# Kernel tuning notes

Hardware: AMD Instinct MI355X
Metric: run time of the kernel (lower is better)

Reference implementation:

```python
import jax, jax.numpy as jnp
import numpy as np

DIM = 1024
HEADS = 16
HEAD_DIM = DIM // HEADS


def setup_inputs() -> dict:
    key = jax.random.key(0)
    ks = jax.random.split(key, 9)
    x = jax.random.normal(ks[0], (2, 2048, DIM), dtype=jnp.float32)
    s = 1.0 / np.sqrt(DIM)
    Wq = jax.random.normal(ks[1], (DIM, DIM), dtype=jnp.float32) * s
    bq = jax.random.normal(ks[2], (DIM,), dtype=jnp.float32) * s
    Wk = jax.random.normal(ks[3], (DIM, DIM), dtype=jnp.float32) * s
    bk = jax.random.normal(ks[4], (DIM,), dtype=jnp.float32) * s
    Wv = jax.random.normal(ks[5], (DIM, DIM), dtype=jnp.float32) * s
    bv = jax.random.normal(ks[6], (DIM,), dtype=jnp.float32) * s
    Wo = jax.random.normal(ks[7], (DIM, DIM), dtype=jnp.float32) * s
    bo = jax.random.normal(ks[8], (DIM,), dtype=jnp.float32) * s
    return {"x": x, "Wq": Wq, "bq": bq, "Wk": Wk, "bk": bk,
            "Wv": Wv, "bv": bv, "Wo": Wo, "bo": bo}


def reference(x, Wq, bq, Wk, bk, Wv, bv, Wo, bo):
    B, S, _ = x.shape
    # projections (torch Linear: x @ W.T + b; here W stored as [in, out])
    q = x @ Wq + bq
    k = x @ Wk + bk  # context = x (self-attention)
    v = x @ Wv + bv
    # [B, H, S, Dh]
    q = q.reshape(B, S, HEADS, HEAD_DIM).transpose(0, 2, 1, 3)
    k = k.reshape(B, S, HEADS, HEAD_DIM).transpose(0, 2, 1, 3)
    v = v.reshape(B, S, HEADS, HEAD_DIM).transpose(0, 2, 1, 3)
    scores = jnp.einsum('bhqd,bhkd->bhqk', q, k) / np.sqrt(HEAD_DIM).astype(np.float32)
    weights = jax.nn.softmax(scores, axis=-1)
    emb = jnp.einsum('bhqk,bhkd->bhqd', weights, v)
    emb = emb.transpose(0, 2, 1, 3).reshape(B, S, DIM)
    return emb @ Wo + bo
```

## Files before the change

kernel.cpp:

```cpp
#include <hip/hip_runtime.h>
#include <hip/hip_bf16.h>
#include <stdint.h>

typedef __attribute__((ext_vector_type(8))) short short8;
typedef __attribute__((ext_vector_type(4))) float f32x4;
typedef __attribute__((ext_vector_type(4))) unsigned int uint4v;

#define DIMW 1024
#define HEADS 16
#define HEAD_DIM 64
#define SEQ 2048
#define BATCH 2
#define MTOK 4096
#define QKVN 3072
#define QKN 2048
#define QSCALE 0.1803368801111204f

typedef const __attribute__((address_space(1))) unsigned int* gas_u32p;
typedef __attribute__((address_space(3))) unsigned int* las_u32p;

static __device__ __forceinline__ void gl_lds16(const void* g, void* l) {
    __builtin_amdgcn_global_load_lds((gas_u32p)g, (las_u32p)l, 16, 0, 0);
}

static __device__ __forceinline__ unsigned short f2bf(float f) {
    unsigned int u = __float_as_uint(f);
    u += 0x7fffu + ((u >> 16) & 1u);
    return (unsigned short)(u >> 16);
}

__global__ void cast_x_kernel(const float* __restrict__ x, unsigned short* __restrict__ out) {
    int i = (blockIdx.x * 256 + threadIdx.x) * 8;
    float4 a = *(const float4*)(x + i);
    float4 b = *(const float4*)(x + i + 4);
    unsigned short t[8] = { f2bf(a.x), f2bf(a.y), f2bf(a.z), f2bf(a.w),
                            f2bf(b.x), f2bf(b.y), f2bf(b.z), f2bf(b.w) };
    *(uint4v*)(out + i) = *(const uint4v*)t;
}

__global__ void prep_w_kernel(const float* __restrict__ Wq, const float* __restrict__ Wk,
                              const float* __restrict__ Wv, const float* __restrict__ Wo,
                              unsigned short* __restrict__ Wqkv_t, unsigned short* __restrict__ Wo_t) {
    __shared__ float tile[64][68];
    int z = blockIdx.z;
    const float* W = (z == 0) ? Wq : (z == 1) ? Wk : (z == 2) ? Wv : Wo;
    unsigned short* out = (z < 3) ? (Wqkv_t + (size_t)z * DIMW * DIMW) : Wo_t;
    int n0 = blockIdx.x * 64, k0 = blockIdx.y * 64;
    int tid = threadIdx.x;
    for (int it = 0; it < 4; ++it) {
        int c = it * 256 + tid;
        int r = c >> 4, cg = c & 15;
        float4 v = *(const float4*)(W + (size_t)(k0 + r) * DIMW + n0 + cg * 4);
        tile[r][cg * 4 + 0] = v.x; tile[r][cg * 4 + 1] = v.y;
        tile[r][cg * 4 + 2] = v.z; tile[r][cg * 4 + 3] = v.w;
    }
    __syncthreads();
    for (int it = 0; it < 2; ++it) {
        int c = it * 256 + tid;
        int n = c >> 3, kg = c & 7;
        unsigned short tmp[8];
        #pragma unroll
        for (int j = 0; j < 8; ++j) tmp[j] = f2bf(tile[kg * 8 + j][n]);
        *(uint4v*)(out + (size_t)(n0 + n) * DIMW + k0 + kg * 8) = *(const uint4v*)tmp;
    }
}

template<int MI, bool QKV3, typename TO>
__global__ __launch_bounds__(256, 3) void gemm_bt_kernel(
    const unsigned short* __restrict__ A, const unsigned short* __restrict__ Bt,
    const float* __restrict__ b0, const float* __restrict__ b1, const float* __restrict__ b2,
    TO* __restrict__ C, unsigned short* __restrict__ Vt, int M, int N, int K, int ldc)
{
    __shared__ __align__(16) unsigned short As[MI * 32 * 32];
    __shared__ __align__(16) unsigned short Bs[128 * 32];
    int tid = threadIdx.x;
    int wave = tid >> 6, lane = tid & 63;
    int lrow = lane & 15, quad = lane >> 4;
    int bm = blockIdx.y * (MI * 32), bn = blockIdx.x * 128;
    int wm = (wave >> 1) * (MI * 16), wn = (wave & 1) * 64;
    int sw = (lrow >> 1) & 3;
    f32x4 acc[MI][4];
    #pragma unroll
    for (int i = 0; i < MI; ++i)
        #pragma unroll
        for (int j = 0; j < 4; ++j) acc[i][j] = (f32x4){0.f, 0.f, 0.f, 0.f};
    const unsigned short* Ap = A + (size_t)bm * K;
    const unsigned short* Bp = Bt + (size_t)bn * K;
    for (int k0 = 0; k0 < K; k0 += 32) {
        __syncthreads();
        #pragma unroll
        for (int it = 0; it < MI / 2; ++it) {
            int c = it * 256 + tid;
            int ch = (c & 3) ^ ((c >> 3) & 3);
            gl_lds16(Ap + (size_t)(c >> 2) * K + k0 + ch * 8, &As[c * 8]);
        }
        #pragma unroll
        for (int it = 0; it < 2; ++it) {
            int c = it * 256 + tid;
            int ch = (c & 3) ^ ((c >> 3) & 3);
            gl_lds16(Bp + (size_t)(c >> 2) * K + k0 + ch * 8, &Bs[c * 8]);
        }
        __syncthreads();
        short8 af[MI], bfr[4];
        #pragma unroll
        for (int mi = 0; mi < MI; ++mi)
            af[mi] = *(const short8*)&As[(wm + mi * 16 + lrow) * 32 + (quad ^ sw) * 8];
        #pragma unroll
        for (int ni = 0; ni < 4; ++ni)
            bfr[ni] = *(const short8*)&Bs[(wn + ni * 16 + lrow) * 32 + (quad ^ sw) * 8];
        #pragma unroll
        for (int mi = 0; mi < MI; ++mi)
            #pragma unroll
            for (int ni = 0; ni < 4; ++ni)
                acc[mi][ni] = __builtin_amdgcn_mfma_f32_16x16x32_bf16(af[mi], bfr[ni], acc[mi][ni], 0, 0, 0);
    }
    #pragma unroll
    for (int ni = 0; ni < 4; ++ni) {
        int n = bn + wn + ni * 16 + lrow;
        float bias, scale;
        int sel = 0;
        if (QKV3) {
            sel = n >> 10;
            const float* bp = (sel == 0) ? b0 : (sel == 1) ? b1 : b2;
            bias = bp[n & 1023];
            scale = (sel == 0) ? QSCALE : 1.0f;
        } else { bias = b0[n]; scale = 1.0f; }
        #pragma unroll
        for (int mi = 0; mi < MI; ++mi) {
            int m0 = bm + wm + mi * 16 + quad * 4;
            if (QKV3 && sel == 2) {
                int vcol = n - 2048;
                int bb = m0 >> 11, s0 = m0 & 2047;
                unsigned short t[4];
                #pragma unroll
                for (int i = 0; i < 4; ++i) t[i] = f2bf(acc[mi][ni][i] + bias);
                *(uint2*)(Vt + ((size_t)(bb * 1024 + vcol)) * SEQ + s0) = *(const uint2*)t;
            } else {
                #pragma unroll
                for (int i = 0; i < 4; ++i) {
                    float val = (acc[mi][ni][i] + bias) * scale;
                    if constexpr (sizeof(TO) == 2) C[(size_t)(m0 + i) * ldc + n] = (TO)f2bf(val);
                    else                           C[(size_t)(m0 + i) * ldc + n] = val;
                }
            }
        }
    }
}

__global__ __launch_bounds__(256, 3) void attn_kernel(
    const unsigned short* __restrict__ Qk, const unsigned short* __restrict__ Vt,
    unsigned short* __restrict__ Op, float* __restrict__ L)
{
    __shared__ __align__(16) unsigned short Ks[128 * 64];
    __shared__ __align__(16) unsigned short Vs[64 * 128];
    __shared__ __align__(16) unsigned short Ps[4][32 * 32];
    int tid = threadIdx.x;
    int wave = tid >> 6, lane = tid & 63;
    int lrow = lane & 15, quad = lane >> 4;
    int h = blockIdx.x, qblk = blockIdx.y;
    int b = blockIdx.z >> 1, split = blockIdx.z & 1;
    int q0 = qblk * 128 + wave * 32;
    const unsigned short* Qbase = Qk + (size_t)(b * SEQ) * QKN + h * 64;
    const unsigned short* Kbase = Qk + (size_t)(b * SEQ) * QKN + 1024 + h * 64;
    const unsigned short* Vtb = Vt + (size_t)(b * 1024 + h * 64) * SEQ;

    short8 qf[2][2];
    #pragma unroll
    for (int mi = 0; mi < 2; ++mi)
        #pragma unroll
        for (int kc = 0; kc < 2; ++kc)
            qf[mi][kc] = *(const short8*)(Qbase + (size_t)(q0 + mi * 16 + lrow) * QKN + kc * 32 + quad * 8);

    f32x4 o[2][4];
    float lrun[2] = {0.f, 0.f};
    #pragma unroll
    for (int mi = 0; mi < 2; ++mi)
        #pragma unroll
        for (int ont = 0; ont < 4; ++ont) o[mi][ont] = (f32x4){0.f, 0.f, 0.f, 0.f};

    int kchunk = ((lane & 7) ^ (lane >> 3)) * 8;
    int swk = lrow & 7;
    int psw = (lrow & 6) << 2;

    auto stageK = [&](int kv) {
        #pragma unroll
        for (int it = 0; it < 4; ++it) {
            int r0 = wave * 32 + it * 8;
            gl_lds16(Kbase + (size_t)(kv + r0 + (lane >> 3)) * QKN + kchunk,
                     &Ks[r0 * 64 + lane * 8]);
        }
    };
    auto stageV = [&](int kv) {
        #pragma unroll
        for (int it = 0; it < 4; ++it) {
            int d0 = wave * 16 + it * 4;
            int vc = ((lane & 15) ^ ((it * 4 + (lane >> 4)) & 15)) * 8;
            gl_lds16(Vtb + (size_t)(d0 + (lane >> 4)) * SEQ + kv + vc,
                     &Vs[d0 * 128 + lane * 8]);
        }
    };

    int kv_lo = split * 1024;
    int kv_end = kv_lo + 1024;

    stageK(kv_lo);
    stageV(kv_lo);

    for (int kv0 = kv_lo; kv0 < kv_end; kv0 += 128) {
        bool has_next = (kv0 + 128) < kv_end;

        asm volatile("s_waitcnt vmcnt(4)" ::: "memory");
        __builtin_amdgcn_sched_barrier(0);
        __builtin_amdgcn_s_barrier();

        int p01[2][8], p23[2][8];
        #pragma unroll
        for (int half = 0; half < 2; ++half) {
            f32x4 s[2][4];
            #pragma unroll
            for (int mi = 0; mi < 2; ++mi)
                #pragma unroll
                for (int nt2 = 0; nt2 < 4; ++nt2) s[mi][nt2] = (f32x4){0.f, 0.f, 0.f, 0.f};
            __builtin_amdgcn_s_setprio(1);
            #pragma unroll
            for (int nt2 = 0; nt2 < 4; ++nt2) {
                int r = (half * 4 + nt2) * 16 + lrow;
                short8 kf0 = *(const short8*)&Ks[r * 64 + (quad ^ swk) * 8];
                short8 kf1 = *(const short8*)&Ks[r * 64 + ((4 + quad) ^ swk) * 8];
                #pragma unroll
                for (int mi = 0; mi < 2; ++mi) {
                    s[mi][nt2] = __builtin_amdgcn_mfma_f32_16x16x32_bf16(kf0, qf[mi][0], s[mi][nt2], 0, 0, 0);
                    s[mi][nt2] = __builtin_amdgcn_mfma_f32_16x16x32_bf16(kf1, qf[mi][1], s[mi][nt2], 0, 0, 0);
                }
            }
            __builtin_amdgcn_s_setprio(0);
            #pragma unroll
            for (int mi = 0; mi < 2; ++mi)
                #pragma unroll
                for (int nt2 = 0; nt2 < 4; ++nt2) {
                    f32x4 p;
                    #pragma unroll
                    for (int c2 = 0; c2 < 4; ++c2) {
                        p[c2] = __builtin_amdgcn_exp2f(s[mi][nt2][c2]);
                        lrun[mi] += p[c2];
                    }
                    __hip_bfloat162 a01 = __float22bfloat162_rn(float2{p[0], p[1]});
                    __hip_bfloat162 a23 = __float22bfloat162_rn(float2{p[2], p[3]});
                    p01[mi][half * 4 + nt2] = *reinterpret_cast<int*>(&a01);
                    p23[mi][half * 4 + nt2] = *reinterpret_cast<int*>(&a23);
                }
        }

        asm volatile("s_waitcnt vmcnt(0)" ::: "memory");
        __builtin_amdgcn_sched_barrier(0);
        __builtin_amdgcn_s_barrier();

        if (has_next) stageK(kv0 + 128);

        #pragma unroll
        for (int kc = 0; kc < 4; ++kc) {
            #pragma unroll
            for (int mi = 0; mi < 2; ++mi)
                #pragma unroll
                for (int h2 = 0; h2 < 2; ++h2) {
                    int nt = kc * 2 + h2;
                    uint2 pk;
                    pk.x = (unsigned int)p01[mi][nt];
                    pk.y = (unsigned int)p23[mi][nt];
                    *(uint2*)&Ps[wave][(mi * 16 + lrow) * 32 + (((h2 * 4 + quad) << 2) ^ psw)] = pk;
                }
            short8 af0 = *(const short8*)&Ps[wave][lrow * 32 + (((quad * 2) << 2) ^ psw)];
            short8 af1 = *(const short8*)&Ps[wave][(16 + lrow) * 32 + (((quad * 2) << 2) ^ psw)];
            __builtin_amdgcn_s_setprio(1);
            #pragma unroll
            for (int ont = 0; ont < 4; ++ont) {
                int rv = ont * 16 + lrow;
                int pos = ((kc * 4 + quad) ^ lrow) * 8;
                short8 vf = *(const short8*)&Vs[rv * 128 + pos];
                o[0][ont] = __builtin_amdgcn_mfma_f32_16x16x32_bf16(af0, vf, o[0][ont], 0, 0, 0);
                o[1][ont] = __builtin_amdgcn_mfma_f32_16x16x32_bf16(af1, vf, o[1][ont], 0, 0, 0);
            }
            __builtin_amdgcn_s_setprio(0);
        }

        __builtin_amdgcn_s_barrier();
        if (has_next) stageV(kv0 + 128);
    }

    #pragma unroll
    for (int mi = 0; mi < 2; ++mi) {
        float l = lrun[mi];
        l += __shfl_xor(l, 16);
        l += __shfl_xor(l, 32);
        #pragma unroll
        for (int ont = 0; ont < 4; ++ont)
            #pragma unroll
            for (int c2 = 0; c2 < 4; ++c2) {
                size_t row = (size_t)((split * 2 + b) * SEQ + q0 + mi * 16 + quad * 4 + c2);
                Op[row * DIMW + h * 64 + ont * 16 + lrow] = f2bf(o[mi][ont][c2]);
            }
        if (quad == 0)
            L[(((size_t)(split * 2 + b) * 16 + h) * SEQ) + q0 + mi * 16 + lrow] = l;
    }
}

__global__ void combine_kernel(const unsigned short* __restrict__ Op,
                               const float* __restrict__ L,
                               unsigned short* __restrict__ Emb)
{
    int e = (blockIdx.x * 256 + threadIdx.x) * 4;
    int row = e >> 10, c = e & 1023, h = c >> 6;
    int b = row >> 11, q = row & 2047;
    float l1 = L[((size_t)(0 + b) * 16 + h) * SEQ + q];
    float l2 = L[((size_t)(2 + b) * 16 + h) * SEQ + q];
    float inv = 1.0f / (l1 + l2);
    uint2 o1 = *(const uint2*)(Op + e);
    uint2 o2 = *(const uint2*)(Op + 4194304 + e);
    unsigned short t[4];
    unsigned int parts1[4] = { o1.x << 16, o1.x & 0xffff0000u, o1.y << 16, o1.y & 0xffff0000u };
    unsigned int parts2[4] = { o2.x << 16, o2.x & 0xffff0000u, o2.y << 16, o2.y & 0xffff0000u };
    #pragma unroll
    for (int j = 0; j < 4; ++j) {
        float f1 = __uint_as_float(parts1[j]);
        float f2 = __uint_as_float(parts2[j]);
        t[j] = f2bf((f1 + f2) * inv);
    }
    *(uint2*)(Emb + e) = *(const uint2*)t;
}

extern "C" void kernel_launch(void* const* d_in, const int* in_sizes, int n_in,
                              void* d_out, int out_size, void* d_ws, size_t ws_size,
                              hipStream_t stream)
{
    const float* x  = (const float*)d_in[0];
    const float* Wq = (const float*)d_in[1];
    const float* bq = (const float*)d_in[2];
    const float* Wk = (const float*)d_in[3];
    const float* bk = (const float*)d_in[4];
    const float* Wv = (const float*)d_in[5];
    const float* bv = (const float*)d_in[6];
    const float* Wo = (const float*)d_in[7];
    const float* bo = (const float*)d_in[8];
    float* out = (float*)d_out;
    char* ws = (char*)d_ws;

    unsigned short* Xbf   = (unsigned short*)(ws);
    unsigned short* Wqkvt = (unsigned short*)(ws + 8388608);
    unsigned short* Wot   = (unsigned short*)(ws + 14680064);
    unsigned short* Qk    = (unsigned short*)(ws + 16777216);
    unsigned short* Vt    = (unsigned short*)(ws + 33554432);
    unsigned short* Emb   = (unsigned short*)(ws + 41943040);
    unsigned short* Op    = (unsigned short*)(ws + 50331648);
    float*          L     = (float*)(ws + 67108864);

    cast_x_kernel<<<2048, 256, 0, stream>>>(x, Xbf);
    prep_w_kernel<<<dim3(16, 16, 4), 256, 0, stream>>>(Wq, Wk, Wv, Wo, Wqkvt, Wot);
    gemm_bt_kernel<4, true, unsigned short><<<dim3(24, 32), 256, 0, stream>>>(
        Xbf, Wqkvt, bq, bk, bv, Qk, Vt, MTOK, QKVN, DIMW, QKN);
    attn_kernel<<<dim3(16, 16, 4), 256, 0, stream>>>(Qk, Vt, Op, L);
    combine_kernel<<<4096, 256, 0, stream>>>(Op, L, Emb);
    gemm_bt_kernel<2, false, float><<<dim3(8, 64), 256, 0, stream>>>(
        Emb, Wot, bo, nullptr, nullptr, out, nullptr, MTOK, DIMW, DIMW, DIMW);
}
```

Before: 203.1 us.

## Keep softmax probabilities in registers and permute V keys to match

Removes the per-wave LDS round trip for the P matrix. The V tile's key order is permuted on load so that the bf16 probabilities already held in registers line up directly as MFMA A operands. V staging changes from direct global-to-LDS loads to a register load followed by a later swizzled LDS write, and the load is issued alongside the next K prefetch. This saves LDS writes, reads and bank traffic per kv step and shrinks LDS use. In exchange it needs more VGPRs for vreg, which may reduce occupancy, and adds a full vmcnt(0) wait before the V write.

```diff
diff --git a/kernel.cpp b/kernel.cpp
--- a/kernel.cpp
+++ b/kernel.cpp
@@ -153,7 +153,6 @@
 {
     __shared__ __align__(16) unsigned short Ks[128 * 64];
     __shared__ __align__(16) unsigned short Vs[64 * 128];
-    __shared__ __align__(16) unsigned short Ps[4][32 * 32];
     int tid = threadIdx.x;
     int wave = tid >> 6, lane = tid & 63;
     int lrow = lane & 15, quad = lane >> 4;
@@ -180,7 +179,6 @@
 
     int kchunk = ((lane & 7) ^ (lane >> 3)) * 8;
     int swk = lrow & 7;
-    int psw = (lrow & 6) << 2;
 
     auto stageK = [&](int kv) {
         #pragma unroll
@@ -190,13 +188,28 @@
                      &Ks[r0 * 64 + lane * 8]);
         }
     };
-    auto stageV = [&](int kv) {
-        #pragma unroll
-        for (int it = 0; it < 4; ++it) {
-            int d0 = wave * 16 + it * 4;
-            int vc = ((lane & 15) ^ ((it * 4 + (lane >> 4)) & 15)) * 8;
-            gl_lds16(Vtb + (size_t)(d0 + (lane >> 4)) * SEQ + kv + vc,
-                     &Vs[d0 * 128 + lane * 8]);
+
+    int vs_s = lane & 15;
+    int vh0 = ((vs_s & 12) << 1) | (vs_s & 3);
+    uint2 vreg[8];
+    auto loadV = [&](int kv) {
+        #pragma unroll
+        for (int r = 0; r < 4; ++r) {
+            int d = wave * 16 + r * 4 + (lane >> 4);
+            const unsigned short* p = Vtb + (size_t)d * SEQ + kv;
+            vreg[r * 2]     = *(const uint2*)(p + vh0 * 4);
+            vreg[r * 2 + 1] = *(const uint2*)(p + (vh0 + 4) * 4);
+        }
+    };
+    auto writeVs = [&]() {
+        #pragma unroll
+        for (int r = 0; r < 4; ++r) {
+            int d = wave * 16 + r * 4 + (lane >> 4);
+            int pos = vs_s ^ (d & 15);
+            uint4v w;
+            w.x = vreg[r * 2].x;     w.y = vreg[r * 2].y;
+            w.z = vreg[r * 2 + 1].x; w.w = vreg[r * 2 + 1].y;
+            *(uint4v*)&Vs[d * 128 + pos * 8] = w;
         }
     };
 
@@ -204,16 +217,17 @@
     int kv_end = kv_lo + 1024;
 
     stageK(kv_lo);
-    stageV(kv_lo);
+    loadV(kv_lo);
+    asm volatile("s_waitcnt vmcnt(0)" ::: "memory");
+    __builtin_amdgcn_sched_barrier(0);
+    writeVs();
 
     for (int kv0 = kv_lo; kv0 < kv_end; kv0 += 128) {
         bool has_next = (kv0 + 128) < kv_end;
 
-        asm volatile("s_waitcnt vmcnt(4)" ::: "memory");
-        __builtin_amdgcn_sched_barrier(0);
         __builtin_amdgcn_s_barrier();
 
-        int p01[2][8], p23[2][8];
+        uint4v pav[2][4];
         #pragma unroll
         for (int half = 0; half < 2; ++half) {
             f32x4 s[2][4];
@@ -238,6 +252,7 @@
             for (int mi = 0; mi < 2; ++mi)
                 #pragma unroll
                 for (int nt2 = 0; nt2 < 4; ++nt2) {
+                    int kt = half * 4 + nt2;
                     f32x4 p;
                     #pragma unroll
                     for (int c2 = 0; c2 < 4; ++c2) {
@@ -246,36 +261,29 @@
                     }
                     __hip_bfloat162 a01 = __float22bfloat162_rn(float2{p[0], p[1]});
                     __hip_bfloat162 a23 = __float22bfloat162_rn(float2{p[2], p[3]});
-                    p01[mi][half * 4 + nt2] = *reinterpret_cast<int*>(&a01);
-                    p23[mi][half * 4 + nt2] = *reinterpret_cast<int*>(&a23);
+                    if (kt & 1) {
+                        pav[mi][kt >> 1].z = *reinterpret_cast<unsigned int*>(&a01);
+                        pav[mi][kt >> 1].w = *reinterpret_cast<unsigned int*>(&a23);
+                    } else {
+                        pav[mi][kt >> 1].x = *reinterpret_cast<unsigned int*>(&a01);
+                        pav[mi][kt >> 1].y = *reinterpret_cast<unsigned int*>(&a23);
+                    }
                 }
         }
 
-        asm volatile("s_waitcnt vmcnt(0)" ::: "memory");
-        __builtin_amdgcn_sched_barrier(0);
         __builtin_amdgcn_s_barrier();
 
-        if (has_next) stageK(kv0 + 128);
+        if (has_next) { stageK(kv0 + 128); loadV(kv0 + 128); }
 
         #pragma unroll
         for (int kc = 0; kc < 4; ++kc) {
-            #pragma unroll
-            for (int mi = 0; mi < 2; ++mi)
-                #pragma unroll
-                for (int h2 = 0; h2 < 2; ++h2) {
-                    int nt = kc * 2 + h2;
-                    uint2 pk;
-                    pk.x = (unsigned int)p01[mi][nt];
-                    pk.y = (unsigned int)p23[mi][nt];
-                    *(uint2*)&Ps[wave][(mi * 16 + lrow) * 32 + (((h2 * 4 + quad) << 2) ^ psw)] = pk;
-                }
-            short8 af0 = *(const short8*)&Ps[wave][lrow * 32 + (((quad * 2) << 2) ^ psw)];
-            short8 af1 = *(const short8*)&Ps[wave][(16 + lrow) * 32 + (((quad * 2) << 2) ^ psw)];
+            short8 af0 = *(short8*)&pav[0][kc];
+            short8 af1 = *(short8*)&pav[1][kc];
+            int pos = ((kc * 4 + quad) ^ lrow) * 8;
             __builtin_amdgcn_s_setprio(1);
             #pragma unroll
             for (int ont = 0; ont < 4; ++ont) {
                 int rv = ont * 16 + lrow;
-                int pos = ((kc * 4 + quad) ^ lrow) * 8;
                 short8 vf = *(const short8*)&Vs[rv * 128 + pos];
                 o[0][ont] = __builtin_amdgcn_mfma_f32_16x16x32_bf16(af0, vf, o[0][ont], 0, 0, 0);
                 o[1][ont] = __builtin_amdgcn_mfma_f32_16x16x32_bf16(af1, vf, o[1][ont], 0, 0, 0);
@@ -284,7 +292,12 @@
         }
 
         __builtin_amdgcn_s_barrier();
-        if (has_next) stageV(kv0 + 128);
+
+        if (has_next) {
+            asm volatile("s_waitcnt vmcnt(0)" ::: "memory");
+            __builtin_amdgcn_sched_barrier(0);
+            writeVs();
+        }
     }
 
     #pragma unroll
```

Result: no change. 202.2 us (-0.5%).
